# Optimization experiments

Hardware: AMD Instinct MI355X
Metric: run time of the kernel (lower is better)

## Reference

```python
import jax, jax.numpy as jnp
import numpy as np

N_NODES = 100000
N_EDGES = 3200000
NEG_SLOPE = 0.2  # PyG GATConv default


def _gat_conv(x, src, dst, W, a_src, a_dst, b, num_nodes):
    # x: [N, Fin]; src/dst: [E'] (self-loops already appended)
    h = x @ W                                   # [N, Fout]
    alpha_src = h @ a_src                       # [N]
    alpha_dst = h @ a_dst                       # [N]
    e = jax.nn.leaky_relu(alpha_src[src] + alpha_dst[dst], NEG_SLOPE)  # [E']
    # segment softmax over incoming edges of each destination node
    e_max = jax.ops.segment_max(e, dst, num_segments=num_nodes)
    e_exp = jnp.exp(e - e_max[dst])
    denom = jax.ops.segment_sum(e_exp, dst, num_segments=num_nodes)
    alpha = e_exp / (denom[dst] + 1e-16)        # [E']
    out = jax.ops.segment_sum(h[src] * alpha[:, None], dst, num_segments=num_nodes)
    return out + b


def setup_inputs() -> dict:
    key = jax.random.key(0)
    ks = jax.random.split(key, 10)
    x = jax.random.normal(ks[0], (N_NODES, 1), jnp.float32)
    edge_index = jax.random.randint(ks[1], (2, N_EDGES), 0, N_NODES, dtype=jnp.int64)
    s1 = 1.0  # glorot-ish scales
    return {
        "x": x,
        "edge_index": edge_index,
        "W1": jax.random.normal(ks[2], (1, 20), jnp.float32) * s1,
        "a_src1": jax.random.normal(ks[3], (20,), jnp.float32) * 0.3,
        "a_dst1": jax.random.normal(ks[4], (20,), jnp.float32) * 0.3,
        "b1": jnp.zeros((20,), jnp.float32),
        "W2": jax.random.normal(ks[5], (20, 20), jnp.float32) * (1.0 / np.sqrt(20.0)),
        "a_src2": jax.random.normal(ks[6], (20,), jnp.float32) * 0.3,
        "a_dst2": jax.random.normal(ks[7], (20,), jnp.float32) * 0.3,
        "b2": jnp.zeros((20,), jnp.float32),
        "Wl": jax.random.normal(ks[8], (20, 1), jnp.float32) * (1.0 / np.sqrt(20.0)),
        "bl": jnp.zeros((1,), jnp.float32),
    }


def reference(x, edge_index, W1, a_src1, a_dst1, b1, W2, a_src2, a_dst2, b2, Wl, bl):
    n = x.shape[0]
    loop = jnp.arange(n, dtype=edge_index.dtype)
    src = jnp.concatenate([edge_index[0], loop])  # add_self_loops=True
    dst = jnp.concatenate([edge_index[1], loop])
    h = _gat_conv(x, src, dst, W1, a_src1, a_dst1, b1, n)
    h = jax.nn.relu(h)
    h = _gat_conv(h, src, dst, W2, a_src2, a_dst2, b2, n)
    h = jax.nn.relu(h)
    return h @ Wl + bl  # [N, 1]
```

## Files before the change

### kernel.cpp

```cpp
#include <hip/hip_runtime.h>
#include <hip/hip_fp16.h>

#define FDIM 20
#define NSLOPE 0.2f
#define BSHIFT 7
#define BSIZE 128
#define BCAP 7168
#define SCAP 4800
#define MAXBUCK 800
#define PGRID 256
#define PCHUNK 12544
#define HSTRIDE 32
#define ABLK 512

__device__ __forceinline__ float lrelu(float v) { return v > 0.f ? v : NSLOPE * v; }

__global__ void k_init(const float* __restrict__ x, const float* __restrict__ W1,
                       const float* __restrict__ a_src, const float* __restrict__ a_dst,
                       float2* __restrict__ PX, float* __restrict__ AD,
                       int* __restrict__ gcur, int N)
{
    int i = blockIdx.x * blockDim.x + threadIdx.x;
    if (i < MAXBUCK) gcur[i] = 0;
    if (i >= N) return;
    float cs = 0.f, cd = 0.f;
#pragma unroll
    for (int f = 0; f < FDIM; ++f) { float w = W1[f]; cs += w * a_src[f]; cd += w * a_dst[f]; }
    float xv = x[i];
    PX[i] = make_float2(xv * cs, xv);
    AD[i] = xv * cd;
}

__global__ void __launch_bounds__(1024)
k_part(const int* __restrict__ ei, int E, int nbuck,
       int* __restrict__ gcur, int* __restrict__ slab)
{
    __shared__ int hist[MAXBUCK];
    __shared__ int base[MAXBUCK];
    __shared__ int loff[MAXBUCK];
    __shared__ int buf[PCHUNK];
    const int tid = threadIdx.x;
    const int chunk = (E + PGRID - 1) / PGRID;
    const int c0 = blockIdx.x * chunk;
    const int c1 = min(c0 + chunk, E);
    for (int t = tid; t < nbuck; t += 1024) hist[t] = 0;
    __syncthreads();
    int i = c0 + 2 * tid;
    for (; i + 1 < c1; i += 2048) {
        int2 d2 = *(const int2*)(ei + E + i);
        atomicAdd(&hist[d2.x >> BSHIFT], 1);
        atomicAdd(&hist[d2.y >> BSHIFT], 1);
    }
    if (i < c1) atomicAdd(&hist[ei[E + i] >> BSHIFT], 1);
    __syncthreads();
    for (int t = tid; t < nbuck; t += 1024) {
        int c = hist[t];
        int r = (c + 15) & ~15;
        base[t] = r ? atomicAdd(gcur + t, r) : 0;
        loff[t] = c;
    }
    __syncthreads();
    for (int o = 1; o < nbuck; o <<= 1) {
        int v = 0;
        if (tid < nbuck && tid >= o) v = loff[tid - o];
        __syncthreads();
        if (tid < nbuck) loff[tid] += v;
        __syncthreads();
    }
    if (tid < nbuck) {
        int ex = loff[tid] - hist[tid];
        loff[tid] = ex;
        hist[tid] = ex;
    }
    __syncthreads();
    i = c0 + 2 * tid;
    for (; i + 1 < c1; i += 2048) {
        int2 s2 = *(const int2*)(ei + i);
        int2 d2 = *(const int2*)(ei + E + i);
        int pA = atomicAdd(&hist[d2.x >> BSHIFT], 1);
        int pB = atomicAdd(&hist[d2.y >> BSHIFT], 1);
        buf[pA] = (s2.x << BSHIFT) | (d2.x & (BSIZE - 1));
        buf[pB] = (s2.y << BSHIFT) | (d2.y & (BSIZE - 1));
    }
    if (i < c1) {
        int s = ei[i], d = ei[E + i];
        int p = atomicAdd(&hist[d >> BSHIFT], 1);
        buf[p] = (s << BSHIFT) | (d & (BSIZE - 1));
    }
    __syncthreads();
    const int wid = tid >> 6, lane = tid & 63;
    for (int t = wid; t < nbuck; t += 16) {
        int ex = loff[t];
        int c = hist[t] - ex;
        int r = (c + 15) & ~15;
        int g = base[t];
        int* dst = slab + (size_t)t * BCAP;
        for (int j = lane; j < r; j += 64) {
            int pos = g + j;
            if (pos < BCAP) dst[pos] = (j < c) ? buf[ex + j] : -1;
        }
    }
}

__global__ void __launch_bounds__(ABLK)
k_agg1(const int* __restrict__ gcur, const int* __restrict__ slab,
       const float2* __restrict__ PX, const float* __restrict__ AD,
       const float* __restrict__ W1, const float* __restrict__ b1,
       const float* __restrict__ W2,
       const float* __restrict__ as2w, const float* __restrict__ ad2w,
       __half* __restrict__ H, float* __restrict__ AD2,
       int* __restrict__ gsedge, int* __restrict__ goff, int N)
{
    __shared__ int sedge[SCAP];
    __shared__ int off[BSIZE + 1], cur[BSIZE];
    __shared__ float sAD[BSIZE];
    __shared__ float sW1[FDIM], sb1[FDIM], sW2[FDIM * FDIM], sas[FDIM], sad[FDIM];
    const int tid = threadIdx.x;
    const int b = blockIdx.x;
    const int dbase = b << BSHIFT;
    if (tid < BSIZE) { int d = dbase + tid; sAD[tid] = (d < N) ? AD[d] : 0.f; }
    for (int t = tid; t < FDIM * FDIM; t += ABLK) sW2[t] = W2[t];
    if (tid >= 480 && tid < 480 + FDIM) {
        int k = tid - 480;
        sW1[k] = W1[k]; sb1[k] = b1[k]; sas[k] = as2w[k]; sad[k] = ad2w[k];
    }
    if (tid < BSIZE + 1) off[tid] = 0;
    __syncthreads();

    const int cnt = min(gcur[b], BCAP);
    const int* sp = slab + (size_t)b * BCAP;
    for (int i = tid; i < cnt; i += ABLK) {
        int e = sp[i];
        if (e >= 0) atomicAdd(&off[(e & (BSIZE - 1)) + 1], 1);
    }
    __syncthreads();
    for (int o = 1; o < BSIZE; o <<= 1) {
        int v = 0;
        if (tid < BSIZE && tid + 1 > o) v = off[tid + 1 - o];
        __syncthreads();
        if (tid < BSIZE) off[tid + 1] += v;
        __syncthreads();
    }
    if (tid < BSIZE) cur[tid] = off[tid];
    __syncthreads();
    for (int i = tid; i < cnt; i += ABLK) {
        int e = sp[i];
        if (e >= 0) {
            int pos = atomicAdd(&cur[e & (BSIZE - 1)], 1);
            sedge[pos] = e >> BSHIFT;
        }
    }
    __syncthreads();

    const int cntT = off[BSIZE];
    for (int i = tid; i < cntT; i += ABLK) gsedge[(size_t)b * SCAP + i] = sedge[i];
    if (tid < BSIZE + 1) goff[b * (BSIZE + 1) + tid] = off[tid];

    const int dl = tid >> 2, sub = tid & 3;
    const float adv = sAD[dl];
    float den = 0.f, sx = 0.f;
    const int e1 = off[dl + 1];
#pragma unroll 2
    for (int j = off[dl] + sub; j < e1; j += 4) {
        int s = sedge[j];
        float2 p = PX[s];
        float w = __expf(lrelu(p.x + adv));
        den += w; sx += w * p.y;
    }
    den += __shfl_xor(den, 1); den += __shfl_xor(den, 2);
    sx  += __shfl_xor(sx, 1);  sx  += __shfl_xor(sx, 2);
    const int d = dbase + dl;
    if (sub == 0 && d < N) {
        float2 p = PX[d];
        float w = __expf(lrelu(p.x + adv));
        den += w; sx += w * p.y;
        float sv = sx / (den + 1e-16f);
        float tk[FDIM];
#pragma unroll
        for (int k = 0; k < FDIM; ++k) {
            float tv = sv * sW1[k] + sb1[k];
            tk[k] = tv > 0.f ? tv : 0.f;
        }
        float pas = 0.f, pad = 0.f;
        __half2* hrow = (__half2*)(H + (size_t)d * HSTRIDE);
#pragma unroll
        for (int f = 0; f < FDIM; f += 2) {
            float h0 = 0.f, h1 = 0.f;
#pragma unroll
            for (int k = 0; k < FDIM; ++k) {
                h0 += tk[k] * sW2[k * FDIM + f];
                h1 += tk[k] * sW2[k * FDIM + f + 1];
            }
            hrow[f >> 1] = __halves2half2(__float2half(h0), __float2half(h1));
            pas += h0 * sas[f] + h1 * sas[f + 1];
            pad += h0 * sad[f] + h1 * sad[f + 1];
        }
        *(float*)(H + (size_t)d * HSTRIDE + FDIM) = pas;
        AD2[d] = pad;
    }
}

__global__ void __launch_bounds__(256)
k_agg2(const int* __restrict__ gsedge, const int* __restrict__ goff,
       const __half* __restrict__ H, const float* __restrict__ AD2,
       const float* __restrict__ b2, const float* __restrict__ Wl,
       const float* __restrict__ bl,
       float* __restrict__ out, int N)
{
    __shared__ int off[65];
    __shared__ float sAD[64];
    __shared__ float sb2[FDIM], sWl[FDIM];
    const int tid = threadIdx.x;
    const int b = blockIdx.x >> 1;
    const int half = blockIdx.x & 1;
    const int dbase = (b << BSHIFT) + (half << 6);
    if (tid < 64) { int d = dbase + tid; sAD[tid] = (d < N) ? AD2[d] : 0.f; }
    if (tid < 65) off[tid] = goff[b * (BSIZE + 1) + (half << 6) + tid];
    if (tid >= 224 && tid < 224 + FDIM) {
        int k = tid - 224;
        sb2[k] = b2[k]; sWl[k] = Wl[k];
    }
    __syncthreads();

    const int* sl = gsedge + (size_t)b * SCAP;
    const int dl = tid >> 2, sub = tid & 3;
    const float adv = sAD[dl];
    float den = 0.f;
    float acc[FDIM];
#pragma unroll
    for (int k = 0; k < FDIM; ++k) acc[k] = 0.f;
    const int e1 = off[dl + 1];
#pragma unroll 2
    for (int j = off[dl] + sub; j < e1; j += 4) {
        int s = sl[j];
        const uint4* rp = (const uint4*)(H + (size_t)s * HSTRIDE);
        uint4 a = rp[0];
        uint4 bb = rp[1];
        uint4 c = rp[2];
        float w = __expf(lrelu(__uint_as_float(c.z) + adv));
        den += w;
        float2 f;
        f = __half22float2(*(__half2*)&a.x);  acc[0]  += w * f.x; acc[1]  += w * f.y;
        f = __half22float2(*(__half2*)&a.y);  acc[2]  += w * f.x; acc[3]  += w * f.y;
        f = __half22float2(*(__half2*)&a.z);  acc[4]  += w * f.x; acc[5]  += w * f.y;
        f = __half22float2(*(__half2*)&a.w);  acc[6]  += w * f.x; acc[7]  += w * f.y;
        f = __half22float2(*(__half2*)&bb.x); acc[8]  += w * f.x; acc[9]  += w * f.y;
        f = __half22float2(*(__half2*)&bb.y); acc[10] += w * f.x; acc[11] += w * f.y;
        f = __half22float2(*(__half2*)&bb.z); acc[12] += w * f.x; acc[13] += w * f.y;
        f = __half22float2(*(__half2*)&bb.w); acc[14] += w * f.x; acc[15] += w * f.y;
        f = __half22float2(*(__half2*)&c.x);  acc[16] += w * f.x; acc[17] += w * f.y;
        f = __half22float2(*(__half2*)&c.y);  acc[18] += w * f.x; acc[19] += w * f.y;
    }
    den += __shfl_xor(den, 1); den += __shfl_xor(den, 2);
#pragma unroll
    for (int k = 0; k < FDIM; ++k) {
        acc[k] += __shfl_xor(acc[k], 1);
        acc[k] += __shfl_xor(acc[k], 2);
    }
    const int d = dbase + dl;
    if (sub == 0 && d < N) {
        const uint4* rp = (const uint4*)(H + (size_t)d * HSTRIDE);
        uint4 a = rp[0], bb = rp[1], c = rp[2];
        float w = __expf(lrelu(__uint_as_float(c.z) + adv));
        den += w;
        float hv[FDIM];
        float2 f;
        f = __half22float2(*(__half2*)&a.x);  hv[0]  = f.x; hv[1]  = f.y;
        f = __half22float2(*(__half2*)&a.y);  hv[2]  = f.x; hv[3]  = f.y;
        f = __half22float2(*(__half2*)&a.z);  hv[4]  = f.x; hv[5]  = f.y;
        f = __half22float2(*(__half2*)&a.w);  hv[6]  = f.x; hv[7]  = f.y;
        f = __half22float2(*(__half2*)&bb.x); hv[8]  = f.x; hv[9]  = f.y;
        f = __half22float2(*(__half2*)&bb.y); hv[10] = f.x; hv[11] = f.y;
        f = __half22float2(*(__half2*)&bb.z); hv[12] = f.x; hv[13] = f.y;
        f = __half22float2(*(__half2*)&bb.w); hv[14] = f.x; hv[15] = f.y;
        f = __half22float2(*(__half2*)&c.x);  hv[16] = f.x; hv[17] = f.y;
        f = __half22float2(*(__half2*)&c.y);  hv[18] = f.x; hv[19] = f.y;
        float inv = 1.f / (den + 1e-16f);
        float r = 0.f;
#pragma unroll
        for (int k = 0; k < FDIM; ++k) {
            float v = (acc[k] + w * hv[k]) * inv + sb2[k];
            v = v > 0.f ? v : 0.f;
            r += v * sWl[k];
        }
        out[d] = r + bl[0];
    }
}

extern "C" void kernel_launch(void* const* d_in, const int* in_sizes, int n_in,
                              void* d_out, int out_size, void* d_ws, size_t ws_size,
                              hipStream_t stream)
{
    const float* x      = (const float*)d_in[0];
    const int*   ei     = (const int*)d_in[1];
    const float* W1     = (const float*)d_in[2];
    const float* a_src1 = (const float*)d_in[3];
    const float* a_dst1 = (const float*)d_in[4];
    const float* b1     = (const float*)d_in[5];
    const float* W2     = (const float*)d_in[6];
    const float* a_src2 = (const float*)d_in[7];
    const float* a_dst2 = (const float*)d_in[8];
    const float* b2     = (const float*)d_in[9];
    const float* Wl     = (const float*)d_in[10];
    const float* bl     = (const float*)d_in[11];
    float* out = (float*)d_out;

    const int N = in_sizes[0];
    const int E = in_sizes[1] / 2;
    const int NBUCK = (N + BSIZE - 1) >> BSHIFT;

    __half* H    = (__half*)d_ws;
    float2* PX   = (float2*)(H + (size_t)N * HSTRIDE);
    float*  AD   = (float*)(PX + N);
    float*  AD2  = AD + N;
    int*  gcur   = (int*)(AD2 + N);
    int*  goff   = gcur + MAXBUCK;
    int*  slab   = goff + MAXBUCK * (BSIZE + 1);
    int*  gsedge = slab + (size_t)MAXBUCK * BCAP;

    const int nb_n = (N + 255) / 256;

    k_init<<<nb_n, 256, 0, stream>>>(x, W1, a_src1, a_dst1, PX, AD, gcur, N);
    k_part<<<PGRID, 1024, 0, stream>>>(ei, E, NBUCK, gcur, slab);
    k_agg1<<<NBUCK, ABLK, 0, stream>>>(gcur, slab, PX, AD, W1, b1, W2,
                                       a_src2, a_dst2, H, AD2, gsedge, goff, N);
    k_agg2<<<2 * NBUCK, 256, 0, stream>>>(gsedge, goff, H, AD2, b2, Wl, bl, out, N);
}
```

Measured before the change: 201.4 us.

## Fuse layer-1 softmax accumulation into bucket scatter and use wave-shuffle prefix scan

The layer-1 edge-weight computation (exp of the leaky-relu score, denominator and weighted-sum accumulation) moves into the loop that scatters edges into per-destination order. It accumulates with shared-memory float atomics, so the separate pass that re-read sedge per destination is gone. The 128-entry offset prefix sum becomes a single-wave shuffle scan instead of a barrier-heavy loop. The cost is contention on shared float atomics for destinations with many edges, and a floating-point summation order that is no longer deterministic.

```diff
diff --git a/kernel.cpp b/kernel.cpp
--- a/kernel.cpp
+++ b/kernel.cpp
@@ -113,12 +113,16 @@
 {
     __shared__ int sedge[SCAP];
     __shared__ int off[BSIZE + 1], cur[BSIZE];
-    __shared__ float sAD[BSIZE];
+    __shared__ float sden[BSIZE], ssx[BSIZE], sAD[BSIZE];
     __shared__ float sW1[FDIM], sb1[FDIM], sW2[FDIM * FDIM], sas[FDIM], sad[FDIM];
     const int tid = threadIdx.x;
     const int b = blockIdx.x;
     const int dbase = b << BSHIFT;
-    if (tid < BSIZE) { int d = dbase + tid; sAD[tid] = (d < N) ? AD[d] : 0.f; }
+    if (tid < BSIZE) {
+        int d = dbase + tid;
+        sAD[tid] = (d < N) ? AD[d] : 0.f;
+        sden[tid] = 0.f; ssx[tid] = 0.f;
+    }
     for (int t = tid; t < FDIM * FDIM; t += ABLK) sW2[t] = W2[t];
     if (tid >= 480 && tid < 480 + FDIM) {
         int k = tid - 480;
@@ -134,20 +138,34 @@
         if (e >= 0) atomicAdd(&off[(e & (BSIZE - 1)) + 1], 1);
     }
     __syncthreads();
-    for (int o = 1; o < BSIZE; o <<= 1) {
-        int v = 0;
-        if (tid < BSIZE && tid + 1 > o) v = off[tid + 1 - o];
-        __syncthreads();
-        if (tid < BSIZE) off[tid + 1] += v;
-        __syncthreads();
-    }
+    if (tid < 64) {
+        int c0 = off[2 * tid + 1];
+        int c1 = off[2 * tid + 2];
+        int p = c0 + c1;
+        int ip = p;
+#pragma unroll
+        for (int o = 1; o < 64; o <<= 1) {
+            int v = __shfl_up(ip, o);
+            if (tid >= o) ip += v;
+        }
+        int ex = ip - p;
+        off[2 * tid + 1] = ex + c0;
+        off[2 * tid + 2] = ex + c0 + c1;
+    }
+    __syncthreads();
     if (tid < BSIZE) cur[tid] = off[tid];
     __syncthreads();
     for (int i = tid; i < cnt; i += ABLK) {
         int e = sp[i];
         if (e >= 0) {
-            int pos = atomicAdd(&cur[e & (BSIZE - 1)], 1);
-            sedge[pos] = e >> BSHIFT;
+            int dl = e & (BSIZE - 1);
+            int s = e >> BSHIFT;
+            int pos = atomicAdd(&cur[dl], 1);
+            sedge[pos] = s;
+            float2 p = PX[s];
+            float w = __expf(lrelu(p.x + sAD[dl]));
+            atomicAdd(&sden[dl], w);
+            atomicAdd(&ssx[dl], w * p.y);
         }
     }
     __syncthreads();
@@ -156,47 +174,37 @@
     for (int i = tid; i < cntT; i += ABLK) gsedge[(size_t)b * SCAP + i] = sedge[i];
     if (tid < BSIZE + 1) goff[b * (BSIZE + 1) + tid] = off[tid];
 
-    const int dl = tid >> 2, sub = tid & 3;
-    const float adv = sAD[dl];
-    float den = 0.f, sx = 0.f;
-    const int e1 = off[dl + 1];
-#pragma unroll 2
-    for (int j = off[dl] + sub; j < e1; j += 4) {
-        int s = sedge[j];
-        float2 p = PX[s];
-        float w = __expf(lrelu(p.x + adv));
-        den += w; sx += w * p.y;
-    }
-    den += __shfl_xor(den, 1); den += __shfl_xor(den, 2);
-    sx  += __shfl_xor(sx, 1);  sx  += __shfl_xor(sx, 2);
-    const int d = dbase + dl;
-    if (sub == 0 && d < N) {
-        float2 p = PX[d];
-        float w = __expf(lrelu(p.x + adv));
-        den += w; sx += w * p.y;
-        float sv = sx / (den + 1e-16f);
-        float tk[FDIM];
-#pragma unroll
-        for (int k = 0; k < FDIM; ++k) {
-            float tv = sv * sW1[k] + sb1[k];
-            tk[k] = tv > 0.f ? tv : 0.f;
-        }
-        float pas = 0.f, pad = 0.f;
-        __half2* hrow = (__half2*)(H + (size_t)d * HSTRIDE);
-#pragma unroll
-        for (int f = 0; f < FDIM; f += 2) {
-            float h0 = 0.f, h1 = 0.f;
+    if (tid < BSIZE) {
+        const int d = dbase + tid;
+        if (d < N) {
+            float2 p = PX[d];
+            float w = __expf(lrelu(p.x + sAD[tid]));
+            float den = sden[tid] + w;
+            float sx  = ssx[tid] + w * p.y;
+            float sv = sx / (den + 1e-16f);
+            float tk[FDIM];
 #pragma unroll
             for (int k = 0; k < FDIM; ++k) {
-                h0 += tk[k] * sW2[k * FDIM + f];
-                h1 += tk[k] * sW2[k * FDIM + f + 1];
+                float tv = sv * sW1[k] + sb1[k];
+                tk[k] = tv > 0.f ? tv : 0.f;
             }
-            hrow[f >> 1] = __halves2half2(__float2half(h0), __float2half(h1));
-            pas += h0 * sas[f] + h1 * sas[f + 1];
-            pad += h0 * sad[f] + h1 * sad[f + 1];
-        }
-        *(float*)(H + (size_t)d * HSTRIDE + FDIM) = pas;
-        AD2[d] = pad;
+            float pas = 0.f, pad = 0.f;
+            __half2* hrow = (__half2*)(H + (size_t)d * HSTRIDE);
+#pragma unroll
+            for (int f = 0; f < FDIM; f += 2) {
+                float h0 = 0.f, h1 = 0.f;
+#pragma unroll
+                for (int k = 0; k < FDIM; ++k) {
+                    h0 += tk[k] * sW2[k * FDIM + f];
+                    h1 += tk[k] * sW2[k * FDIM + f + 1];
+                }
+                hrow[f >> 1] = __halves2half2(__float2half(h0), __float2half(h1));
+                pas += h0 * sas[f] + h1 * sas[f + 1];
+                pad += h0 * sad[f] + h1 * sad[f + 1];
+            }
+            *(float*)(H + (size_t)d * HSTRIDE + FDIM) = pas;
+            AD2[d] = pad;
+        }
     }
 }
 
```

After: 221.6 us. 1.1x slower.
